# Optimization experiments

Measured on AMD Instinct MI355X. Metric: run time of the kernel, lower is better.

The kernel has to match this reference:

```python
import jax, jax.numpy as jnp
import numpy as np

B, P, H, W = 64, 50000, 512, 512


def setup_inputs() -> dict:
    key = jax.random.key(0)
    ks = jax.random.split(key, 6)
    x = jax.random.normal(ks[0], (B, 1, H, W), dtype=jnp.float32)
    x_A = jax.random.randint(ks[1], (B, P), 0, W, dtype=jnp.int32)
    y_A = jax.random.randint(ks[2], (B, P), 0, H, dtype=jnp.int32)
    x_B = jax.random.randint(ks[3], (B, P), 0, W, dtype=jnp.int32)
    y_B = jax.random.randint(ks[4], (B, P), 0, H, dtype=jnp.int32)
    # ordinal relation in {-1, 0, 1}: -1/+1 = ordered pair, 0 = equal depth
    gt = jax.random.randint(ks[5], (B, P), -1, 2).astype(jnp.float32)
    return {"x": x, "x_A": x_A, "y_A": y_A, "x_B": x_B, "y_B": y_B, "gt": gt}


def reference(x, x_A, y_A, x_B, y_B, gt):
    # x: [B,1,H,W] predicted depth; gather z values at sparse point pairs.
    img = x[:, 0]                              # [B,H,W]
    b = jnp.arange(B)[:, None]                 # [B,1] batch index for gather
    z_A = img[b, y_A, x_A]                     # [B,P]
    z_B = img[b, y_B, x_B]                     # [B,P]
    d = z_A - z_B
    mask = jnp.abs(gt)                         # 1 for ordered pairs, 0 for equal
    # ranking loss log(1+exp(-gt*d)) for ordered pairs, (d)^2 for equal pairs
    loss = mask * jnp.log1p(jnp.exp(-gt * d)) + (1.0 - mask) * d * d
    n_point_total = B * P
    return jnp.sum(loss) / n_point_total
```

## Files before the change

kernel.cpp:

```cpp
#include <hip/hip_runtime.h>

#define THREADS 256
#define BLOCKS_PER_XCD 192
#define NXCD 8
#define NBLOCKS (BLOCKS_PER_XCD * NXCD)

typedef int   intx4   __attribute__((ext_vector_type(4)));
typedef float floatx4 __attribute__((ext_vector_type(4)));

__global__ __launch_bounds__(THREADS) void rdc_kernel(
    const float* __restrict__ x,
    const int*   __restrict__ xA,
    const int*   __restrict__ yA,
    const int*   __restrict__ xB,
    const int*   __restrict__ yB,
    const float* __restrict__ gt,
    float* __restrict__ out,
    float inv_n)
{
    const int P4  = 12500;
    const int BPX = 8;
    const int HW  = 512 * 512;

    const int xcd = blockIdx.x & 7;
    const int lb  = blockIdx.x >> 3;
    const int tlocal = lb * THREADS + threadIdx.x;
    const int nthreads_xcd = BLOCKS_PER_XCD * THREADS;
    const int total = BPX * P4;

    float acc = 0.0f;
    for (int j = tlocal; j < total; j += nthreads_xcd) {
        const int bl = j / P4;
        const int i  = j - bl * P4;
        const int b  = xcd * BPX + bl;
        const int v  = b * P4 + i;

        const intx4  xa = __builtin_nontemporal_load((const intx4*)xA + v);
        const intx4  ya = __builtin_nontemporal_load((const intx4*)yA + v);
        const intx4  xb = __builtin_nontemporal_load((const intx4*)xB + v);
        const intx4  yb = __builtin_nontemporal_load((const intx4*)yB + v);
        const floatx4 g = __builtin_nontemporal_load((const floatx4*)gt + v);

        const float* __restrict__ img = x + (size_t)b * HW;

        #pragma unroll
        for (int k = 0; k < 4; ++k) {
            float zA = img[(ya[k] << 9) + xa[k]];
            float zB = img[(yb[k] << 9) + xb[k]];
            float d  = zA - zB;
            float gi = g[k];

            float t  = -gi * d;
            float sp = fmaxf(t, 0.0f) + log1pf(__expf(-fabsf(t)));
            float m  = fabsf(gi);
            acc += m * sp + (1.0f - m) * d * d;
        }
    }

    #pragma unroll
    for (int off = 32; off > 0; off >>= 1)
        acc += __shfl_down(acc, off, 64);

    __shared__ float wsum[THREADS / 64];
    const int lane = threadIdx.x & 63;
    const int wid  = threadIdx.x >> 6;
    if (lane == 0) wsum[wid] = acc;
    __syncthreads();
    if (threadIdx.x == 0) {
        float s = 0.0f;
        #pragma unroll
        for (int i2 = 0; i2 < THREADS / 64; ++i2) s += wsum[i2];
        atomicAdd(out, s * inv_n);
    }
}

extern "C" void kernel_launch(void* const* d_in, const int* in_sizes, int n_in,
                              void* d_out, int out_size, void* d_ws, size_t ws_size,
                              hipStream_t stream) {
    const float* x  = (const float*)d_in[0];
    const int*   xA = (const int*)d_in[1];
    const int*   yA = (const int*)d_in[2];
    const int*   xB = (const int*)d_in[3];
    const int*   yB = (const int*)d_in[4];
    const float* gt = (const float*)d_in[5];
    float* out = (float*)d_out;

    const int n = in_sizes[1];
    const float inv_n = 1.0f / (float)n;

    hipMemsetAsync(out, 0, sizeof(float), stream);
    rdc_kernel<<<NBLOCKS, THREADS, 0, stream>>>(x, xA, yA, xB, yB, gt, out, inv_n);
}
```

Baseline: 170.0 us.

## Assign eight pairs per thread in a single pass and batch all gathers

Replaces the grid-stride loop with a fixed mapping where each thread handles exactly eight point pairs (two vec4 loads per array), resizing the grid to 196 blocks per XCD so the work is covered in one pass. All sixteen image gathers are issued before any loss math, raising memory-level parallelism per thread. This removes loop overhead and the per-iteration division, but ties correctness to hard-coded sizes and raises register use.

```diff
diff --git a/kernel.cpp b/kernel.cpp
--- a/kernel.cpp
+++ b/kernel.cpp
@@ -1,7 +1,7 @@
 #include <hip/hip_runtime.h>
 
 #define THREADS 256
-#define BLOCKS_PER_XCD 192
+#define BLOCKS_PER_XCD 196
 #define NXCD 8
 #define NBLOCKS (BLOCKS_PER_XCD * NXCD)
 
@@ -18,38 +18,46 @@
     float* __restrict__ out,
     float inv_n)
 {
-    const int P4  = 12500;
-    const int BPX = 8;
+    const int UPB = 6250;
     const int HW  = 512 * 512;
 
     const int xcd = blockIdx.x & 7;
     const int lb  = blockIdx.x >> 3;
     const int tlocal = lb * THREADS + threadIdx.x;
-    const int nthreads_xcd = BLOCKS_PER_XCD * THREADS;
-    const int total = BPX * P4;
 
     float acc = 0.0f;
-    for (int j = tlocal; j < total; j += nthreads_xcd) {
-        const int bl = j / P4;
-        const int i  = j - bl * P4;
-        const int b  = xcd * BPX + bl;
-        const int v  = b * P4 + i;
+    if (tlocal < 8 * UPB) {
+        const int bl = tlocal / UPB;
+        const int i  = tlocal - bl * UPB;
+        const int b  = xcd * 8 + bl;
+        const int v2 = (b * UPB + i) * 2;
 
-        const intx4  xa = __builtin_nontemporal_load((const intx4*)xA + v);
-        const intx4  ya = __builtin_nontemporal_load((const intx4*)yA + v);
-        const intx4  xb = __builtin_nontemporal_load((const intx4*)xB + v);
-        const intx4  yb = __builtin_nontemporal_load((const intx4*)yB + v);
-        const floatx4 g = __builtin_nontemporal_load((const floatx4*)gt + v);
+        const intx4  xa0 = __builtin_nontemporal_load((const intx4*)xA + v2);
+        const intx4  xa1 = __builtin_nontemporal_load((const intx4*)xA + v2 + 1);
+        const intx4  ya0 = __builtin_nontemporal_load((const intx4*)yA + v2);
+        const intx4  ya1 = __builtin_nontemporal_load((const intx4*)yA + v2 + 1);
+        const intx4  xb0 = __builtin_nontemporal_load((const intx4*)xB + v2);
+        const intx4  xb1 = __builtin_nontemporal_load((const intx4*)xB + v2 + 1);
+        const intx4  yb0 = __builtin_nontemporal_load((const intx4*)yB + v2);
+        const intx4  yb1 = __builtin_nontemporal_load((const intx4*)yB + v2 + 1);
+        const floatx4 g0 = __builtin_nontemporal_load((const floatx4*)gt + v2);
+        const floatx4 g1 = __builtin_nontemporal_load((const floatx4*)gt + v2 + 1);
 
         const float* __restrict__ img = x + (size_t)b * HW;
 
+        float zA[8], zB[8];
         #pragma unroll
         for (int k = 0; k < 4; ++k) {
-            float zA = img[(ya[k] << 9) + xa[k]];
-            float zB = img[(yb[k] << 9) + xb[k]];
-            float d  = zA - zB;
-            float gi = g[k];
+            zA[k]     = img[(ya0[k] << 9) + xa0[k]];
+            zA[k + 4] = img[(ya1[k] << 9) + xa1[k]];
+            zB[k]     = img[(yb0[k] << 9) + xb0[k]];
+            zB[k + 4] = img[(yb1[k] << 9) + xb1[k]];
+        }
 
+        #pragma unroll
+        for (int k = 0; k < 8; ++k) {
+            float gi = (k < 4) ? g0[k] : g1[k - 4];
+            float d  = zA[k] - zB[k];
             float t  = -gi * d;
             float sp = fmaxf(t, 0.0f) + log1pf(__expf(-fabsf(t)));
             float m  = fabsf(gi);
```

Measured after the change: 172.3 us. About the same (+1.4%).
